# Optimization experiments

Hardware: AMD Instinct MI355X
Metric: run time of the kernel (lower is better)

The kernel has to match this reference:

```python
import jax, jax.numpy as jnp
import numpy as np

B, S, H, NH, HD = 2, 2048, 2048, 16, 128


def _bit_linear(x, w):
    """Ternary STE BitLinear: absmean scaling, round/clamp, fp matmul, rescale."""
    eps = 1e-5
    wn = w / (jnp.abs(w).mean() + eps)
    # straight-through estimator: forward uses quantized weights, grad flows to wn
    wq = wn + jax.lax.stop_gradient(jnp.clip(jnp.round(wn), -1.0, 1.0) - wn)
    y = x @ wq.T
    scale = w.shape[1]  # in_features
    Qb = 128.0  # 2**(8-1)
    return jnp.clip(y / scale * Qb, -Qb, Qb)


def _rotate_half(x):
    x1, x2 = jnp.split(x, 2, axis=-1)
    return jnp.concatenate([-x2, x1], axis=-1)


def setup_inputs() -> dict:
    key = jax.random.key(0)
    k1, k2, k3 = jax.random.split(key, 3)
    x = jax.random.normal(k1, (B, S, H), dtype=jnp.float32)
    w_qkv = jax.random.normal(k2, (3 * H, H), dtype=jnp.float32) * 0.02
    w_o = jax.random.normal(k3, (H, H), dtype=jnp.float32) * 0.02
    # realistic RoPE table [2, S, HD]
    inv_freq = 1.0 / (10000.0 ** (jnp.arange(0, HD, 2, dtype=jnp.float32) / HD))
    freqs = jnp.arange(S, dtype=jnp.float32)[:, None] * inv_freq[None, :]
    emb = jnp.concatenate([freqs, freqs], axis=-1)  # [S, HD]
    rotary = jnp.stack([jnp.cos(emb), jnp.sin(emb)], axis=0)
    return {"x": x, "rotary": rotary, "w_qkv": w_qkv, "w_o": w_o}


def reference(x, rotary, w_qkv, w_o):
    qkv = _bit_linear(x, w_qkv)  # [B, S, 3H]
    q, k, v = jnp.split(qkv, 3, axis=-1)
    q = q.reshape(B, S, NH, HD)
    k = k.reshape(B, S, NH, HD)
    v = v.reshape(B, S, NH, HD)
    cos = rotary[0][None, :, None, :]  # [1, S, 1, HD]
    sin = rotary[1][None, :, None, :]
    q = q * cos + _rotate_half(q) * sin
    k = k * cos + _rotate_half(k) * sin
    # [B, NH, S, HD]
    q, k, v = (t.transpose(0, 2, 1, 3) for t in (q, k, v))
    scores = jnp.einsum("bhqd,bhkd->bhqk", q, k) / np.sqrt(HD).astype(np.float32)
    causal = jnp.tril(jnp.ones((S, S), dtype=bool))
    scores = jnp.where(causal[None, None], scores, -jnp.inf)
    attn = jax.nn.softmax(scores, axis=-1)
    y = jnp.einsum("bhqk,bhkd->bhqd", attn, v)
    y = y.transpose(0, 2, 1, 3).reshape(B, S, H)
    return _bit_linear(y, w_o)
```

## Files before the change

### kernel.cpp

```cpp
#include <hip/hip_runtime.h>
#include <hip/hip_bf16.h>
#include <stdint.h>

#define B_   2
#define S_   2048
#define H_   2048
#define NH_  16
#define HD_  128
#define MTOK 4096
#define NQKV 6144

typedef unsigned short u16;
typedef __attribute__((ext_vector_type(8))) __bf16 bf16x8;
typedef __attribute__((ext_vector_type(4))) float f32x4;
typedef __attribute__((ext_vector_type(16))) float f32x16;

static __device__ __forceinline__ float bf2f(u16 u){
  union { uint32_t i; float f; } v; v.i = ((uint32_t)u) << 16; return v.f;
}
static __device__ __forceinline__ u16 f2bf(float f){
  union { float f; uint32_t i; } v; v.f = f;
  uint32_t r = v.i + 0x7FFFu + ((v.i >> 16) & 1u);
  return (u16)(r >> 16);
}
static __device__ __forceinline__ uint32_t cvt_pk_bf16(float lo, float hi){
  uint32_t r;
  asm("v_cvt_pk_bf16_f32 %0, %1, %2" : "=v"(r) : "v"(lo), "v"(hi));
  return r;
}
static __device__ __forceinline__ void pl32swap(uint32_t &a, uint32_t &b){
  asm volatile("v_permlane32_swap_b32 %0, %1" : "+v"(a), "+v"(b));
}

__device__ __forceinline__ void gload_lds16(const void* g, void* l){
  __builtin_amdgcn_global_load_lds((const __attribute__((address_space(1))) void*)g,
                                   (__attribute__((address_space(3))) void*)l, 16, 0, 0);
}

__global__ void absum_kernel(const float* __restrict__ w, int n, float* __restrict__ partial){
  __shared__ float sm[256];
  float s = 0.f;
  for (int i = blockIdx.x*256 + threadIdx.x; i < n; i += gridDim.x*256)
    s += fabsf(w[i]);
  sm[threadIdx.x] = s; __syncthreads();
  for (int st = 128; st > 0; st >>= 1){
    if ((int)threadIdx.x < st) sm[threadIdx.x] += sm[threadIdx.x + st];
    __syncthreads();
  }
  if (threadIdx.x == 0) partial[blockIdx.x] = sm[0];
}

__global__ void finalize_kernel(const float* __restrict__ p1, const float* __restrict__ p2,
                                float* __restrict__ scales){
  __shared__ double sm[256];
  int t = threadIdx.x;
  double s = (double)p1[t] + (double)p1[t+256] + (double)p1[t+512] + (double)p1[t+768];
  sm[t] = s; __syncthreads();
  for (int st = 128; st > 0; st >>= 1){ if (t < st) sm[t] += sm[t+st]; __syncthreads(); }
  if (t == 0) scales[0] = (float)(1.0 / (sm[0] / (double)(3*H_*H_) + 1e-5));
  __syncthreads();
  s = (double)p2[t] + (double)p2[t+256] + (double)p2[t+512] + (double)p2[t+768];
  sm[t] = s; __syncthreads();
  for (int st = 128; st > 0; st >>= 1){ if (t < st) sm[t] += sm[t+st]; __syncthreads(); }
  if (t == 0) scales[1] = (float)(1.0 / (sm[0] / (double)(H_*H_) + 1e-5));
}

__global__ void quantcast_kernel(const float* __restrict__ w_qkv, const float* __restrict__ w_o,
                                 const float* __restrict__ x, u16* __restrict__ wqkvq,
                                 u16* __restrict__ woq, u16* __restrict__ xb,
                                 const float* __restrict__ scales){
  const int n1 = 3*H_*H_, n2 = H_*H_, n3 = MTOK*H_;
  float inv0 = scales[0], inv1 = scales[1];
  for (int i = blockIdx.x*256 + threadIdx.x; i < n1 + n2 + n3; i += gridDim.x*256){
    if (i < n1){
      float q = rintf(w_qkv[i] * inv0);
      wqkvq[i] = f2bf(fminf(1.f, fmaxf(-1.f, q)));
    } else if (i < n1 + n2){
      int j = i - n1;
      float q = rintf(w_o[j] * inv1);
      woq[j] = f2bf(fminf(1.f, fmaxf(-1.f, q)));
    } else {
      int j = i - n1 - n2;
      xb[j] = f2bf(x[j]);
    }
  }
}

__global__ __launch_bounds__(512, 4) void gemmqkv_kernel(const u16* __restrict__ A,
    const u16* __restrict__ Bw, u16* __restrict__ qb, u16* __restrict__ kb, u16* __restrict__ vtb)
{
  const int M = MTOK, N = NQKV, K = H_;
  __shared__ u16 As[128*32];
  __shared__ u16 Bs[256*32];
  int nbn = N >> 8;
  int nb_tot = (M >> 7) * nbn;
  int bid = blockIdx.x;
  int chunk = nb_tot >> 3;
  bid = (bid & 7) * chunk + (bid >> 3);
  int bm = bid / nbn, bn = bid % nbn;
  int m0 = bm << 7, n0 = bn << 8;
  int tid = threadIdx.x;
  int lane = tid & 63, wid = tid >> 6;
  int wr = wid >> 2, wc = wid & 3;
  int lg = lane >> 4, lr = lane & 15;

  const u16* Ab = A + (size_t)m0 * K;
  const u16* Bb = Bw + (size_t)n0 * K;
  int srow = tid >> 2;
  int scol = (tid & 3) << 3;

  f32x4 acc[4][4];
  #pragma unroll
  for (int i = 0; i < 4; i++)
    #pragma unroll
    for (int j = 0; j < 4; j++) acc[i][j] = f32x4{0.f,0.f,0.f,0.f};

  for (int k0 = 0; k0 < K; k0 += 32){
    gload_lds16(Ab + (size_t)srow*K        + k0 + scol, As + tid*8);
    gload_lds16(Bb + (size_t)srow*K        + k0 + scol, Bs + tid*8);
    gload_lds16(Bb + (size_t)(srow+128)*K  + k0 + scol, Bs + 4096 + tid*8);
    __syncthreads();
    bf16x8 af[4], bfr[4];
    #pragma unroll
    for (int mi = 0; mi < 4; mi++) af[mi]  = *(const bf16x8*)(As + ((wr*64 + mi*16 + lr)*32 + lg*8));
    #pragma unroll
    for (int ni = 0; ni < 4; ni++) bfr[ni] = *(const bf16x8*)(Bs + ((wc*64 + ni*16 + lr)*32 + lg*8));
    #pragma unroll
    for (int mi = 0; mi < 4; mi++)
      #pragma unroll
      for (int ni = 0; ni < 4; ni++)
        acc[mi][ni] = __builtin_amdgcn_mfma_f32_16x16x32_bf16(af[mi], bfr[ni], acc[mi][ni], 0, 0, 0);
    __syncthreads();
  }

  #pragma unroll
  for (int mi = 0; mi < 4; mi++){
    #pragma unroll
    for (int ni = 0; ni < 4; ni++){
      int ncol = n0 + wc*64 + ni*16 + lr;
      #pragma unroll
      for (int r = 0; r < 4; r++){
        int m = m0 + wr*64 + mi*16 + lg*4 + r;
        float v = acc[mi][ni][r] * 0.0625f;
        v = fminf(128.f, fmaxf(-128.f, v));
        int b = m >> 11, s = m & 2047;
        int part = ncol >> 11, c = ncol & 2047;
        int h = c >> 7, d = c & 127;
        int bh = b*NH_ + h;
        u16 bv = f2bf(v);
        if (part == 0)      qb[((bh*S_ + s) << 7) + d] = bv;
        else if (part == 1) kb[((bh*S_ + s) << 7) + d] = bv;
        else                vtb[((bh*HD_ + d) << 11) + s] = bv;
      }
    }
  }
}

__global__ __launch_bounds__(256, 4) void gemmo_kernel(const u16* __restrict__ A,
    const u16* __restrict__ Bw, float* __restrict__ outf)
{
  const int M = MTOK, N = H_, K = H_;
  __shared__ u16 As[128*32];
  __shared__ u16 Bs[128*32];
  int nbn = N >> 7;
  int nb_tot = (M >> 7) * nbn;
  int bid = blockIdx.x;
  int chunk = nb_tot >> 3;
  bid = (bid & 7) * chunk + (bid >> 3);
  int bm = bid / nbn, bn = bid % nbn;
  int m0 = bm << 7, n0 = bn << 7;
  int tid = threadIdx.x;
  int lane = tid & 63, wid = tid >> 6;
  int wr = wid >> 1, wc = wid & 1;
  int lg = lane >> 4, lr = lane & 15;

  const u16* Ab = A + m0 * K;
  const u16* Bb = Bw + n0 * K;
  int srow = tid >> 2;
  int scol = (tid & 3) << 3;

  f32x4 acc[4][4];
  #pragma unroll
  for (int i = 0; i < 4; i++)
    #pragma unroll
    for (int j = 0; j < 4; j++) acc[i][j] = f32x4{0.f,0.f,0.f,0.f};

  for (int k0 = 0; k0 < K; k0 += 32){
    gload_lds16(Ab + srow*K      + k0 + scol, As + tid*8);
    gload_lds16(Ab + (srow+64)*K + k0 + scol, As + 2048 + tid*8);
    gload_lds16(Bb + srow*K      + k0 + scol, Bs + tid*8);
    gload_lds16(Bb + (srow+64)*K + k0 + scol, Bs + 2048 + tid*8);
    __syncthreads();
    bf16x8 af[4], bfr[4];
    #pragma unroll
    for (int mi = 0; mi < 4; mi++) af[mi]  = *(const bf16x8*)(As + ((wr*64 + mi*16 + lr)*32 + lg*8));
    #pragma unroll
    for (int ni = 0; ni < 4; ni++) bfr[ni] = *(const bf16x8*)(Bs + ((wc*64 + ni*16 + lr)*32 + lg*8));
    #pragma unroll
    for (int mi = 0; mi < 4; mi++)
      #pragma unroll
      for (int ni = 0; ni < 4; ni++)
        acc[mi][ni] = __builtin_amdgcn_mfma_f32_16x16x32_bf16(af[mi], bfr[ni], acc[mi][ni], 0, 0, 0);
    __syncthreads();
  }

  #pragma unroll
  for (int mi = 0; mi < 4; mi++){
    #pragma unroll
    for (int ni = 0; ni < 4; ni++){
      int ncol = n0 + wc*64 + ni*16 + lr;
      #pragma unroll
      for (int r = 0; r < 4; r++){
        int m = m0 + wr*64 + mi*16 + lg*4 + r;
        float v = acc[mi][ni][r] * 0.0625f;
        v = fminf(128.f, fmaxf(-128.f, v));
        outf[(size_t)m*N + ncol] = v;
      }
    }
  }
}

__global__ void rope_kernel(u16* __restrict__ qb, u16* __restrict__ kb, const float* __restrict__ rot){
  int i = blockIdx.x*256 + threadIdx.x;
  int d = i & 63;
  int s = (i >> 6) & 2047;
  int bh = (i >> 17) & 31;
  u16* buf = (i >> 22) ? kb : qb;
  int base = (bh*S_ + s)*HD_;
  float c  = rot[s*HD_ + d];
  float sn = rot[S_*HD_ + s*HD_ + d];
  float x1 = bf2f(buf[base + d]);
  float x2 = bf2f(buf[base + d + 64]);
  buf[base + d]      = f2bf(x1*c - x2*sn);
  buf[base + d + 64] = f2bf(x2*c + x1*sn);
}

__global__ __launch_bounds__(256) void attn_kernel(const u16* __restrict__ qb,
    const u16* __restrict__ kb, const u16* __restrict__ vtb, u16* __restrict__ ao)
{
  __shared__ alignas(16) u16 Ks[2][4096];
  __shared__ alignas(16) u16 Vs[2][4096];

  int bid = blockIdx.x;
  int sbid = (bid & 7)*64 + (bid >> 3);
  int bh = sbid >> 4;
  int bq = 15 - (sbid & 15);
  int tid = threadIdx.x;
  int wid = tid >> 6, lane = tid & 63;
  int l31 = lane & 31, hl = lane >> 5;
  int q0 = bq * 128;
  int qw = q0 + wid*32;
  int q  = qw + l31;

  const u16* Qp = qb + (size_t)(bh*S_ + qw)*HD_;
  const u16* Kp = kb + (size_t)bh*S_*HD_;
  const u16* Vt = vtb + (size_t)bh*HD_*S_;

  bf16x8 qf[8];
  #pragma unroll
  for (int t = 0; t < 8; t++)
    qf[t] = *(const bf16x8*)(Qp + l31*HD_ + t*16 + hl*8);

  f32x16 o[4];
  #pragma unroll
  for (int i = 0; i < 4; i++)
    #pragma unroll
    for (int j = 0; j < 16; j++) o[i][j] = 0.f;
  float m_r = -1e30f, l_r = 0.f;
  const float sm_scale = 0.08838834764831845f;

  auto STAGE = [&](int buf, int kt2){
    int t0 = wid*2;
    gload_lds16(Kp + (size_t)(kt2 + l31)*HD_ + (t0  )*16 + hl*8, &Ks[buf][((t0  )*64 + lane)*8]);
    gload_lds16(Kp + (size_t)(kt2 + l31)*HD_ + (t0+1)*16 + hl*8, &Ks[buf][((t0+1)*64 + lane)*8]);
    int v0 = wid*2, v1 = wid*2 + 1;
    gload_lds16(Vt + (size_t)((v0&3)*32 + l31)*S_ + kt2 + (v0>>2)*16 + hl*8, &Vs[buf][(v0*64 + lane)*8]);
    gload_lds16(Vt + (size_t)((v1&3)*32 + l31)*S_ + kt2 + (v1>>2)*16 + hl*8, &Vs[buf][(v1*64 + lane)*8]);
  };

  int n_it = 4*bq + 4;
  STAGE(0, 0);
  int cur = 0, kt = 0;
  for (int it = 0; it < n_it; ++it, kt += 32){
    if (it + 1 < n_it){
      STAGE(cur ^ 1, kt + 32);
      asm volatile("s_waitcnt vmcnt(4)" ::: "memory");
    } else {
      asm volatile("s_waitcnt vmcnt(0)" ::: "memory");
    }
    __builtin_amdgcn_sched_barrier(0);
    __builtin_amdgcn_s_barrier();

    if (kt <= qw){
      f32x16 sa;
      #pragma unroll
      for (int j = 0; j < 16; j++) sa[j] = 0.f;
      #pragma unroll
      for (int t = 0; t < 8; t++){
        bf16x8 kf = *(const bf16x8*)(&Ks[cur][(t*64 + lane)*8]);
        sa = __builtin_amdgcn_mfma_f32_32x32x16_bf16(kf, qf[t], sa, 0, 0, 0);
      }

      float sv[16];
      if (kt == qw){
        #pragma unroll
        for (int r = 0; r < 16; r++){
          int key = kt + (r&3) + 8*(r>>2) + 4*hl;
          sv[r] = (key > q) ? -1e30f : sa[r]*sm_scale;
        }
      } else {
        #pragma unroll
        for (int r = 0; r < 16; r++) sv[r] = sa[r]*sm_scale;
      }

      float pm = sv[0];
      #pragma unroll
      for (int r = 1; r < 16; r++) pm = fmaxf(pm, sv[r]);
      pm = fmaxf(pm, __shfl_xor(pm, 32));
      if (!__all(pm - m_r <= 8.f)){
        float mn = fmaxf(m_r, pm);
        float scl = __expf(m_r - mn);
        m_r = mn; l_r *= scl;
        #pragma unroll
        for (int i = 0; i < 4; i++)
          #pragma unroll
          for (int j = 0; j < 16; j++) o[i][j] *= scl;
      }
      float p[16];
      #pragma unroll
      for (int r = 0; r < 16; r++) p[r] = __expf(sv[r] - m_r);
      float ts = 0.f;
      #pragma unroll
      for (int r = 0; r < 16; r++) ts += p[r];
      ts += __shfl_xor(ts, 32);
      l_r += ts;

      uint32_t a0 = cvt_pk_bf16(p[0],  p[1]),  a1 = cvt_pk_bf16(p[2],  p[3]);
      uint32_t a2 = cvt_pk_bf16(p[4],  p[5]),  a3 = cvt_pk_bf16(p[6],  p[7]);
      uint32_t b0 = cvt_pk_bf16(p[8],  p[9]),  b1 = cvt_pk_bf16(p[10], p[11]);
      uint32_t b2 = cvt_pk_bf16(p[12], p[13]), b3 = cvt_pk_bf16(p[14], p[15]);
      pl32swap(a0, a2); pl32swap(a1, a3);
      pl32swap(b0, b2); pl32swap(b1, b3);
      union { uint32_t u[4]; bf16x8 v; } pf0, pf1;
      pf0.u[0]=a0; pf0.u[1]=a1; pf0.u[2]=a2; pf0.u[3]=a3;
      pf1.u[0]=b0; pf1.u[1]=b1; pf1.u[2]=b2; pf1.u[3]=b3;

      #pragma unroll
      for (int db = 0; db < 4; db++){
        bf16x8 vf0 = *(const bf16x8*)(&Vs[cur][((0*4 + db)*64 + lane)*8]);
        o[db] = __builtin_amdgcn_mfma_f32_32x32x16_bf16(vf0, pf0.v, o[db], 0, 0, 0);
        bf16x8 vf1 = *(const bf16x8*)(&Vs[cur][((1*4 + db)*64 + lane)*8]);
        o[db] = __builtin_amdgcn_mfma_f32_32x32x16_bf16(vf1, pf1.v, o[db], 0, 0, 0);
      }
      asm volatile("s_waitcnt lgkmcnt(0)" ::: "memory");
    }
    __builtin_amdgcn_sched_barrier(0);
    __builtin_amdgcn_s_barrier();
    cur ^= 1;
  }

  float inv = 1.f / l_r;
  int b = bh >> 4, hh = bh & 15;
  u16* orow = ao + (size_t)(b*S_ + q)*H_ + hh*HD_;
  #pragma unroll
  for (int db = 0; db < 4; db++){
    #pragma unroll
    for (int g = 0; g < 4; g++){
      ushort4 pk4;
      pk4.x = f2bf(o[db][4*g+0]*inv);
      pk4.y = f2bf(o[db][4*g+1]*inv);
      pk4.z = f2bf(o[db][4*g+2]*inv);
      pk4.w = f2bf(o[db][4*g+3]*inv);
      *(ushort4*)(orow + db*32 + g*8 + hl*4) = pk4;
    }
  }
}

extern "C" void kernel_launch(void* const* d_in, const int* in_sizes, int n_in,
                              void* d_out, int out_size, void* d_ws, size_t ws_size,
                              hipStream_t stream) {
  const float* x      = (const float*)d_in[0];
  const float* rotary = (const float*)d_in[1];
  const float* w_qkv  = (const float*)d_in[2];
  const float* w_o    = (const float*)d_in[3];
  float* out = (float*)d_out;

  char* wsb = (char*)d_ws;
  float* part_qkv = (float*)wsb;
  float* part_o   = part_qkv + 1024;
  float* scales   = part_o + 1024;
  size_t off = 16384;
  u16* xb    = (u16*)(wsb + off); off += (size_t)MTOK*H_*2;
  u16* wqkvq = (u16*)(wsb + off); off += (size_t)NQKV*H_*2;
  u16* woq   = (u16*)(wsb + off); off += (size_t)H_*H_*2;
  u16* qbuf  = (u16*)(wsb + off); off += (size_t)B_*NH_*S_*HD_*2;
  u16* kbuf  = (u16*)(wsb + off); off += (size_t)B_*NH_*S_*HD_*2;
  u16* vtb   = (u16*)(wsb + off); off += (size_t)B_*NH_*S_*HD_*2;
  u16* ao    = (u16*)(wsb + off); off += (size_t)MTOK*H_*2;

  absum_kernel<<<1024, 256, 0, stream>>>(w_qkv, 3*H_*H_, part_qkv);
  absum_kernel<<<1024, 256, 0, stream>>>(w_o, H_*H_, part_o);
  finalize_kernel<<<1, 256, 0, stream>>>(part_qkv, part_o, scales);
  quantcast_kernel<<<2048, 256, 0, stream>>>(w_qkv, w_o, x, wqkvq, woq, xb, scales);

  gemmqkv_kernel<<<(MTOK/128)*(NQKV/256), 512, 0, stream>>>(xb, wqkvq, qbuf, kbuf, vtb);
  rope_kernel<<<(2*B_*NH_*S_*64)/256, 256, 0, stream>>>(qbuf, kbuf, rotary);
  attn_kernel<<<B_*NH_*(S_/128), 256, 0, stream>>>(qbuf, kbuf, vtb, ao);
  gemmo_kernel<<<(MTOK/128)*(H_/128), 256, 0, stream>>>(ao, woq, out);
}
```

Baseline: 382.8 us.

## Double-buffer LDS tiles in QKV and output projection GEMMs

Both GEMM kernels now keep two LDS buffers and issue the global-to-LDS loads for the next K tile before computing on the current one. The aim is to overlap global memory latency with MFMA work and drop one barrier per iteration. It doubles shared memory per block, which may lower occupancy, and the single remaining barrier depends on how gload_lds completion is waited on (vmcnt) before the data is read.

```diff
diff --git a/kernel.cpp b/kernel.cpp
--- a/kernel.cpp
+++ b/kernel.cpp
@@ -90,8 +90,8 @@
     const u16* __restrict__ Bw, u16* __restrict__ qb, u16* __restrict__ kb, u16* __restrict__ vtb)
 {
   const int M = MTOK, N = NQKV, K = H_;
-  __shared__ u16 As[128*32];
-  __shared__ u16 Bs[256*32];
+  __shared__ u16 As[2][128*32];
+  __shared__ u16 Bs[2][256*32];
   int nbn = N >> 8;
   int nb_tot = (M >> 7) * nbn;
   int bid = blockIdx.x;
@@ -115,22 +115,30 @@
     #pragma unroll
     for (int j = 0; j < 4; j++) acc[i][j] = f32x4{0.f,0.f,0.f,0.f};
 
-  for (int k0 = 0; k0 < K; k0 += 32){
-    gload_lds16(Ab + (size_t)srow*K        + k0 + scol, As + tid*8);
-    gload_lds16(Bb + (size_t)srow*K        + k0 + scol, Bs + tid*8);
-    gload_lds16(Bb + (size_t)(srow+128)*K  + k0 + scol, Bs + 4096 + tid*8);
-    __syncthreads();
+  auto STAGE = [&](int buf, int k0){
+    gload_lds16(Ab + (size_t)srow*K       + k0 + scol, As[buf] + tid*8);
+    gload_lds16(Bb + (size_t)srow*K       + k0 + scol, Bs[buf] + tid*8);
+    gload_lds16(Bb + (size_t)(srow+128)*K + k0 + scol, Bs[buf] + 4096 + tid*8);
+  };
+
+  int NT = K >> 5;
+  STAGE(0, 0);
+  __syncthreads();
+  int buf = 0;
+  for (int t = 0; t < NT; t++){
+    if (t + 1 < NT) STAGE(buf ^ 1, (t + 1) << 5);
     bf16x8 af[4], bfr[4];
     #pragma unroll
-    for (int mi = 0; mi < 4; mi++) af[mi]  = *(const bf16x8*)(As + ((wr*64 + mi*16 + lr)*32 + lg*8));
-    #pragma unroll
-    for (int ni = 0; ni < 4; ni++) bfr[ni] = *(const bf16x8*)(Bs + ((wc*64 + ni*16 + lr)*32 + lg*8));
+    for (int mi = 0; mi < 4; mi++) af[mi]  = *(const bf16x8*)(As[buf] + ((wr*64 + mi*16 + lr)*32 + lg*8));
+    #pragma unroll
+    for (int ni = 0; ni < 4; ni++) bfr[ni] = *(const bf16x8*)(Bs[buf] + ((wc*64 + ni*16 + lr)*32 + lg*8));
     #pragma unroll
     for (int mi = 0; mi < 4; mi++)
       #pragma unroll
       for (int ni = 0; ni < 4; ni++)
         acc[mi][ni] = __builtin_amdgcn_mfma_f32_16x16x32_bf16(af[mi], bfr[ni], acc[mi][ni], 0, 0, 0);
     __syncthreads();
+    buf ^= 1;
   }
 
   #pragma unroll
@@ -160,8 +168,8 @@
     const u16* __restrict__ Bw, float* __restrict__ outf)
 {
   const int M = MTOK, N = H_, K = H_;
-  __shared__ u16 As[128*32];
-  __shared__ u16 Bs[128*32];
+  __shared__ u16 As[2][128*32];
+  __shared__ u16 Bs[2][128*32];
   int nbn = N >> 7;
   int nb_tot = (M >> 7) * nbn;
   int bid = blockIdx.x;
@@ -185,23 +193,31 @@
     #pragma unroll
     for (int j = 0; j < 4; j++) acc[i][j] = f32x4{0.f,0.f,0.f,0.f};
 
-  for (int k0 = 0; k0 < K; k0 += 32){
-    gload_lds16(Ab + srow*K      + k0 + scol, As + tid*8);
-    gload_lds16(Ab + (srow+64)*K + k0 + scol, As + 2048 + tid*8);
-    gload_lds16(Bb + srow*K      + k0 + scol, Bs + tid*8);
-    gload_lds16(Bb + (srow+64)*K + k0 + scol, Bs + 2048 + tid*8);
-    __syncthreads();
+  auto STAGE = [&](int buf, int k0){
+    gload_lds16(Ab + (size_t)srow*K      + k0 + scol, As[buf] + tid*8);
+    gload_lds16(Ab + (size_t)(srow+64)*K + k0 + scol, As[buf] + 2048 + tid*8);
+    gload_lds16(Bb + (size_t)srow*K      + k0 + scol, Bs[buf] + tid*8);
+    gload_lds16(Bb + (size_t)(srow+64)*K + k0 + scol, Bs[buf] + 2048 + tid*8);
+  };
+
+  int NT = K >> 5;
+  STAGE(0, 0);
+  __syncthreads();
+  int buf = 0;
+  for (int t = 0; t < NT; t++){
+    if (t + 1 < NT) STAGE(buf ^ 1, (t + 1) << 5);
     bf16x8 af[4], bfr[4];
     #pragma unroll
-    for (int mi = 0; mi < 4; mi++) af[mi]  = *(const bf16x8*)(As + ((wr*64 + mi*16 + lr)*32 + lg*8));
-    #pragma unroll
-    for (int ni = 0; ni < 4; ni++) bfr[ni] = *(const bf16x8*)(Bs + ((wc*64 + ni*16 + lr)*32 + lg*8));
+    for (int mi = 0; mi < 4; mi++) af[mi]  = *(const bf16x8*)(As[buf] + ((wr*64 + mi*16 + lr)*32 + lg*8));
+    #pragma unroll
+    for (int ni = 0; ni < 4; ni++) bfr[ni] = *(const bf16x8*)(Bs[buf] + ((wc*64 + ni*16 + lr)*32 + lg*8));
     #pragma unroll
     for (int mi = 0; mi < 4; mi++)
       #pragma unroll
       for (int ni = 0; ni < 4; ni++)
         acc[mi][ni] = __builtin_amdgcn_mfma_f32_16x16x32_bf16(af[mi], bfr[ni], acc[mi][ni], 0, 0, 0);
     __syncthreads();
+    buf ^= 1;
   }
 
   #pragma unroll
```

Measured after the change: 394.9 us. 3.1% more time.

## Double attention key tile to 64 per iteration and add MFMA priority hints

Applied to the files above, without the earlier changes.

The flash-attention kernel now stages 64 keys per iteration instead of 32, doubling the LDS buffers, and computes two 32x32 score tiles with a joint online-softmax update. This halves the number of barrier and wait round trips and softmax rescale checks per key. s_setprio is placed around the MFMA sections to favour matrix issue. In exchange it uses more LDS and registers per block, which may lower occupancy, and adds extra branching for the half-masked diagonal tile.

```diff
diff --git a/kernel.cpp b/kernel.cpp
--- a/kernel.cpp
+++ b/kernel.cpp
@@ -238,8 +238,8 @@
 __global__ __launch_bounds__(256) void attn_kernel(const u16* __restrict__ qb,
     const u16* __restrict__ kb, const u16* __restrict__ vtb, u16* __restrict__ ao)
 {
-  __shared__ alignas(16) u16 Ks[2][4096];
-  __shared__ alignas(16) u16 Vs[2][4096];
+  __shared__ alignas(16) u16 Ks[2][8192];
+  __shared__ alignas(16) u16 Vs[2][8192];
 
   int bid = blockIdx.x;
   int sbid = (bid & 7)*64 + (bid >> 3);
@@ -270,52 +270,65 @@
   const float sm_scale = 0.08838834764831845f;
 
   auto STAGE = [&](int buf, int kt2){
-    int t0 = wid*2;
-    gload_lds16(Kp + (size_t)(kt2 + l31)*HD_ + (t0  )*16 + hl*8, &Ks[buf][((t0  )*64 + lane)*8]);
-    gload_lds16(Kp + (size_t)(kt2 + l31)*HD_ + (t0+1)*16 + hl*8, &Ks[buf][((t0+1)*64 + lane)*8]);
-    int v0 = wid*2, v1 = wid*2 + 1;
-    gload_lds16(Vt + (size_t)((v0&3)*32 + l31)*S_ + kt2 + (v0>>2)*16 + hl*8, &Vs[buf][(v0*64 + lane)*8]);
-    gload_lds16(Vt + (size_t)((v1&3)*32 + l31)*S_ + kt2 + (v1>>2)*16 + hl*8, &Vs[buf][(v1*64 + lane)*8]);
+    #pragma unroll
+    for (int j = 0; j < 4; j++){
+      int f = wid*4 + j;
+      gload_lds16(Kp + (size_t)(kt2 + (f>>3)*32 + l31)*HD_ + (f&7)*16 + hl*8,
+                  &Ks[buf][f*512 + lane*8]);
+      gload_lds16(Vt + (size_t)((f&3)*32 + l31)*S_ + kt2 + (f>>2)*16 + hl*8,
+                  &Vs[buf][f*512 + lane*8]);
+    }
   };
 
-  int n_it = 4*bq + 4;
+  int n_it = 2*bq + 2;
   STAGE(0, 0);
   int cur = 0, kt = 0;
-  for (int it = 0; it < n_it; ++it, kt += 32){
+  for (int it = 0; it < n_it; ++it, kt += 64){
     if (it + 1 < n_it){
-      STAGE(cur ^ 1, kt + 32);
-      asm volatile("s_waitcnt vmcnt(4)" ::: "memory");
+      STAGE(cur ^ 1, kt + 64);
+      asm volatile("s_waitcnt vmcnt(8)" ::: "memory");
     } else {
       asm volatile("s_waitcnt vmcnt(0)" ::: "memory");
     }
     __builtin_amdgcn_sched_barrier(0);
     __builtin_amdgcn_s_barrier();
 
-    if (kt <= qw){
-      f32x16 sa;
-      #pragma unroll
-      for (int j = 0; j < 16; j++) sa[j] = 0.f;
+    if (kt < qw + 32){
+      bool half2 = kt < qw;
+      f32x16 sa0, sa1;
+      #pragma unroll
+      for (int j = 0; j < 16; j++){ sa0[j] = 0.f; sa1[j] = 0.f; }
+      __builtin_amdgcn_s_setprio(1);
       #pragma unroll
       for (int t = 0; t < 8; t++){
         bf16x8 kf = *(const bf16x8*)(&Ks[cur][(t*64 + lane)*8]);
-        sa = __builtin_amdgcn_mfma_f32_32x32x16_bf16(kf, qf[t], sa, 0, 0, 0);
-      }
-
-      float sv[16];
-      if (kt == qw){
+        sa0 = __builtin_amdgcn_mfma_f32_32x32x16_bf16(kf, qf[t], sa0, 0, 0, 0);
+      }
+      if (half2){
+        #pragma unroll
+        for (int t = 0; t < 8; t++){
+          bf16x8 kf = *(const bf16x8*)(&Ks[cur][((8 + t)*64 + lane)*8]);
+          sa1 = __builtin_amdgcn_mfma_f32_32x32x16_bf16(kf, qf[t], sa1, 0, 0, 0);
+        }
+      }
+      __builtin_amdgcn_s_setprio(0);
+
+      float sv[32];
+      if (kt + 63 <= qw){
+        #pragma unroll
+        for (int r = 0; r < 16; r++){ sv[r] = sa0[r]*sm_scale; sv[16+r] = sa1[r]*sm_scale; }
+      } else {
         #pragma unroll
         for (int r = 0; r < 16; r++){
-          int key = kt + (r&3) + 8*(r>>2) + 4*hl;
-          sv[r] = (key > q) ? -1e30f : sa[r]*sm_scale;
+          int crow = (r&3) + 8*(r>>2) + 4*hl;
+          sv[r]    = (kt + crow > q)               ? -1e30f : sa0[r]*sm_scale;
+          sv[16+r] = (!half2 || kt + 32 + crow > q) ? -1e30f : sa1[r]*sm_scale;
         }
-      } else {
-        #pragma unroll
-        for (int r = 0; r < 16; r++) sv[r] = sa[r]*sm_scale;
       }
 
       float pm = sv[0];
       #pragma unroll
-      for (int r = 1; r < 16; r++) pm = fmaxf(pm, sv[r]);
+      for (int r = 1; r < 32; r++) pm = fmaxf(pm, sv[r]);
       pm = fmaxf(pm, __shfl_xor(pm, 32));
       if (!__all(pm - m_r <= 8.f)){
         float mn = fmaxf(m_r, pm);
@@ -326,32 +339,44 @@
           #pragma unroll
           for (int j = 0; j < 16; j++) o[i][j] *= scl;
       }
-      float p[16];
-      #pragma unroll
-      for (int r = 0; r < 16; r++) p[r] = __expf(sv[r] - m_r);
+      float p[32];
+      #pragma unroll
+      for (int r = 0; r < 32; r++) p[r] = __expf(sv[r] - m_r);
       float ts = 0.f;
       #pragma unroll
-      for (int r = 0; r < 16; r++) ts += p[r];
+      for (int r = 0; r < 32; r++) ts += p[r];
       ts += __shfl_xor(ts, 32);
       l_r += ts;
 
-      uint32_t a0 = cvt_pk_bf16(p[0],  p[1]),  a1 = cvt_pk_bf16(p[2],  p[3]);
-      uint32_t a2 = cvt_pk_bf16(p[4],  p[5]),  a3 = cvt_pk_bf16(p[6],  p[7]);
-      uint32_t b0 = cvt_pk_bf16(p[8],  p[9]),  b1 = cvt_pk_bf16(p[10], p[11]);
-      uint32_t b2 = cvt_pk_bf16(p[12], p[13]), b3 = cvt_pk_bf16(p[14], p[15]);
-      pl32swap(a0, a2); pl32swap(a1, a3);
-      pl32swap(b0, b2); pl32swap(b1, b3);
-      union { uint32_t u[4]; bf16x8 v; } pf0, pf1;
-      pf0.u[0]=a0; pf0.u[1]=a1; pf0.u[2]=a2; pf0.u[3]=a3;
-      pf1.u[0]=b0; pf1.u[1]=b1; pf1.u[2]=b2; pf1.u[3]=b3;
-
+      union { uint32_t u[4]; bf16x8 v; } pf[4];
+      #pragma unroll
+      for (int g = 0; g < 4; g++){
+        uint32_t u0 = cvt_pk_bf16(p[8*g+0], p[8*g+1]);
+        uint32_t u1 = cvt_pk_bf16(p[8*g+2], p[8*g+3]);
+        uint32_t u2 = cvt_pk_bf16(p[8*g+4], p[8*g+5]);
+        uint32_t u3 = cvt_pk_bf16(p[8*g+6], p[8*g+7]);
+        pl32swap(u0, u2); pl32swap(u1, u3);
+        pf[g].u[0]=u0; pf[g].u[1]=u1; pf[g].u[2]=u2; pf[g].u[3]=u3;
+      }
+
+      __builtin_amdgcn_s_setprio(1);
       #pragma unroll
       for (int db = 0; db < 4; db++){
-        bf16x8 vf0 = *(const bf16x8*)(&Vs[cur][((0*4 + db)*64 + lane)*8]);
-        o[db] = __builtin_amdgcn_mfma_f32_32x32x16_bf16(vf0, pf0.v, o[db], 0, 0, 0);
-        bf16x8 vf1 = *(const bf16x8*)(&Vs[cur][((1*4 + db)*64 + lane)*8]);
-        o[db] = __builtin_amdgcn_mfma_f32_32x32x16_bf16(vf1, pf1.v, o[db], 0, 0, 0);
-      }
+        bf16x8 v0 = *(const bf16x8*)(&Vs[cur][((0*4 + db)*64 + lane)*8]);
+        o[db] = __builtin_amdgcn_mfma_f32_32x32x16_bf16(v0, pf[0].v, o[db], 0, 0, 0);
+        bf16x8 v1 = *(const bf16x8*)(&Vs[cur][((1*4 + db)*64 + lane)*8]);
+        o[db] = __builtin_amdgcn_mfma_f32_32x32x16_bf16(v1, pf[1].v, o[db], 0, 0, 0);
+      }
+      if (half2){
+        #pragma unroll
+        for (int db = 0; db < 4; db++){
+          bf16x8 v2 = *(const bf16x8*)(&Vs[cur][((2*4 + db)*64 + lane)*8]);
+          o[db] = __builtin_amdgcn_mfma_f32_32x32x16_bf16(v2, pf[2].v, o[db], 0, 0, 0);
+          bf16x8 v3 = *(const bf16x8*)(&Vs[cur][((3*4 + db)*64 + lane)*8]);
+          o[db] = __builtin_amdgcn_mfma_f32_32x32x16_bf16(v3, pf[3].v, o[db], 0, 0, 0);
+        }
+      }
+      __builtin_amdgcn_s_setprio(0);
       asm volatile("s_waitcnt lgkmcnt(0)" ::: "memory");
     }
     __builtin_amdgcn_sched_barrier(0);
```

Measured after the change: 421.4 us. 10.1% more time.

## Switch attention to 16x16x32 MFMA with 64-query blocks and doubled grid

Applied to the files above, without the earlier changes.

Rewrites the attention kernel to use 16x16x32 bf16 MFMA tiles, with each wave handling 16 queries and each block 64 queries, which doubles the number of blocks. Shuffles replace the permlane32 swap to rearrange P into the B-operand layout. The aim is finer causal granularity, less wasted diagonal work and better occupancy and load balance. In exchange, K/V tiles are loaded from global memory twice as often relative to the compute done, and the shuffles add cross-lane overhead.

```diff
diff --git a/kernel.cpp b/kernel.cpp
--- a/kernel.cpp
+++ b/kernel.cpp
@@ -13,7 +13,6 @@
 typedef unsigned short u16;
 typedef __attribute__((ext_vector_type(8))) __bf16 bf16x8;
 typedef __attribute__((ext_vector_type(4))) float f32x4;
-typedef __attribute__((ext_vector_type(16))) float f32x16;
 
 static __device__ __forceinline__ float bf2f(u16 u){
   union { uint32_t i; float f; } v; v.i = ((uint32_t)u) << 16; return v.f;
@@ -27,9 +26,6 @@
   uint32_t r;
   asm("v_cvt_pk_bf16_f32 %0, %1, %2" : "=v"(r) : "v"(lo), "v"(hi));
   return r;
-}
-static __device__ __forceinline__ void pl32swap(uint32_t &a, uint32_t &b){
-  asm volatile("v_permlane32_swap_b32 %0, %1" : "+v"(a), "+v"(b));
 }
 
 __device__ __forceinline__ void gload_lds16(const void* g, void* l){
@@ -242,43 +238,46 @@
   __shared__ alignas(16) u16 Vs[2][4096];
 
   int bid = blockIdx.x;
-  int sbid = (bid & 7)*64 + (bid >> 3);
-  int bh = sbid >> 4;
-  int bq = 15 - (sbid & 15);
+  int sbid = (bid & 7)*128 + (bid >> 3);
+  int bh = sbid >> 5;
+  int bq = 31 - (sbid & 31);
   int tid = threadIdx.x;
   int wid = tid >> 6, lane = tid & 63;
-  int l31 = lane & 31, hl = lane >> 5;
-  int q0 = bq * 128;
-  int qw = q0 + wid*32;
-  int q  = qw + l31;
+  int lg = lane >> 4, lr = lane & 15;
+  int q0 = bq * 64;
+  int qw = q0 + wid*16;
+  int q  = qw + lr;
 
   const u16* Qp = qb + (size_t)(bh*S_ + qw)*HD_;
   const u16* Kp = kb + (size_t)bh*S_*HD_;
   const u16* Vt = vtb + (size_t)bh*HD_*S_;
 
-  bf16x8 qf[8];
-  #pragma unroll
-  for (int t = 0; t < 8; t++)
-    qf[t] = *(const bf16x8*)(Qp + l31*HD_ + t*16 + hl*8);
-
-  f32x16 o[4];
-  #pragma unroll
-  for (int i = 0; i < 4; i++)
-    #pragma unroll
-    for (int j = 0; j < 16; j++) o[i][j] = 0.f;
+  bf16x8 qf[4];
+  #pragma unroll
+  for (int kk = 0; kk < 4; kk++)
+    qf[kk] = *(const bf16x8*)(Qp + lr*HD_ + kk*32 + lg*8);
+
+  f32x4 o[8];
+  #pragma unroll
+  for (int i = 0; i < 8; i++) o[i] = f32x4{0.f,0.f,0.f,0.f};
   float m_r = -1e30f, l_r = 0.f;
   const float sm_scale = 0.08838834764831845f;
 
+  int srcA = ((((lg&1)<<1) | (lg>>1)) << 4) + lr;
+  int srcB = srcA ^ 16;
+
   auto STAGE = [&](int buf, int kt2){
-    int t0 = wid*2;
-    gload_lds16(Kp + (size_t)(kt2 + l31)*HD_ + (t0  )*16 + hl*8, &Ks[buf][((t0  )*64 + lane)*8]);
-    gload_lds16(Kp + (size_t)(kt2 + l31)*HD_ + (t0+1)*16 + hl*8, &Ks[buf][((t0+1)*64 + lane)*8]);
-    int v0 = wid*2, v1 = wid*2 + 1;
-    gload_lds16(Vt + (size_t)((v0&3)*32 + l31)*S_ + kt2 + (v0>>2)*16 + hl*8, &Vs[buf][(v0*64 + lane)*8]);
-    gload_lds16(Vt + (size_t)((v1&3)*32 + l31)*S_ + kt2 + (v1>>2)*16 + hl*8, &Vs[buf][(v1*64 + lane)*8]);
+    #pragma unroll
+    for (int j = 0; j < 2; j++){
+      int f = wid*2 + j;
+      gload_lds16(Kp + (size_t)(kt2 + (f>>2)*16 + lr)*HD_ + (f&3)*32 + lg*8,
+                  &Ks[buf][(f*64 + lane)*8]);
+      gload_lds16(Vt + (size_t)(f*16 + lr)*S_ + kt2 + lg*8,
+                  &Vs[buf][(f*64 + lane)*8]);
+    }
   };
 
-  int n_it = 4*bq + 4;
+  int n_it = 2*bq + 2;
   STAGE(0, 0);
   int cur = 0, kt = 0;
   for (int it = 0; it < n_it; ++it, kt += 32){
@@ -291,66 +290,71 @@
     __builtin_amdgcn_sched_barrier(0);
     __builtin_amdgcn_s_barrier();
 
-    if (kt <= qw){
-      f32x16 sa;
-      #pragma unroll
-      for (int j = 0; j < 16; j++) sa[j] = 0.f;
-      #pragma unroll
-      for (int t = 0; t < 8; t++){
-        bf16x8 kf = *(const bf16x8*)(&Ks[cur][(t*64 + lane)*8]);
-        sa = __builtin_amdgcn_mfma_f32_32x32x16_bf16(kf, qf[t], sa, 0, 0, 0);
-      }
-
-      float sv[16];
-      if (kt == qw){
+    if (kt <= qw + 15){
+      f32x4 s0 = f32x4{0.f,0.f,0.f,0.f}, s1 = f32x4{0.f,0.f,0.f,0.f};
+      #pragma unroll
+      for (int kk = 0; kk < 4; kk++){
+        bf16x8 ka  = *(const bf16x8*)(&Ks[cur][((kk    )*64 + lane)*8]);
+        bf16x8 kb2 = *(const bf16x8*)(&Ks[cur][((4 + kk)*64 + lane)*8]);
+        s0 = __builtin_amdgcn_mfma_f32_16x16x32_bf16(ka,  qf[kk], s0, 0, 0, 0);
+        s1 = __builtin_amdgcn_mfma_f32_16x16x32_bf16(kb2, qf[kk], s1, 0, 0, 0);
+      }
+
+      float sv[8];
+      if (kt + 31 <= qw){
         #pragma unroll
-        for (int r = 0; r < 16; r++){
-          int key = kt + (r&3) + 8*(r>>2) + 4*hl;
-          sv[r] = (key > q) ? -1e30f : sa[r]*sm_scale;
-        }
+        for (int r = 0; r < 4; r++){ sv[r] = s0[r]*sm_scale; sv[4+r] = s1[r]*sm_scale; }
       } else {
         #pragma unroll
-        for (int r = 0; r < 16; r++) sv[r] = sa[r]*sm_scale;
-      }
-
-      float pm = sv[0];
-      #pragma unroll
-      for (int r = 1; r < 16; r++) pm = fmaxf(pm, sv[r]);
+        for (int r = 0; r < 4; r++){
+          sv[r]   = (kt + 4*lg + r      > q) ? -1e30f : s0[r]*sm_scale;
+          sv[4+r] = (kt + 16 + 4*lg + r > q) ? -1e30f : s1[r]*sm_scale;
+        }
+      }
+
+      float pm = fmaxf(fmaxf(fmaxf(sv[0],sv[1]), fmaxf(sv[2],sv[3])),
+                       fmaxf(fmaxf(sv[4],sv[5]), fmaxf(sv[6],sv[7])));
+      pm = fmaxf(pm, __shfl_xor(pm, 16));
       pm = fmaxf(pm, __shfl_xor(pm, 32));
       if (!__all(pm - m_r <= 8.f)){
         float mn = fmaxf(m_r, pm);
         float scl = __expf(m_r - mn);
         m_r = mn; l_r *= scl;
         #pragma unroll
-        for (int i = 0; i < 4; i++)
+        for (int i = 0; i < 8; i++)
           #pragma unroll
-          for (int j = 0; j < 16; j++) o[i][j] *= scl;
-      }
-      float p[16];
-      #pragma unroll
-      for (int r = 0; r < 16; r++) p[r] = __expf(sv[r] - m_r);
-      float ts = 0.f;
-      #pragma unroll
-      for (int r = 0; r < 16; r++) ts += p[r];
+          for (int j = 0; j < 4; j++) o[i][j] *= scl;
+      }
+      float p[8];
+      #pragma unroll
+      for (int i = 0; i < 8; i++) p[i] = __expf(sv[i] - m_r);
+      float ts = ((p[0]+p[1]) + (p[2]+p[3])) + ((p[4]+p[5]) + (p[6]+p[7]));
+      ts += __shfl_xor(ts, 16);
       ts += __shfl_xor(ts, 32);
       l_r += ts;
 
-      uint32_t a0 = cvt_pk_bf16(p[0],  p[1]),  a1 = cvt_pk_bf16(p[2],  p[3]);
-      uint32_t a2 = cvt_pk_bf16(p[4],  p[5]),  a3 = cvt_pk_bf16(p[6],  p[7]);
-      uint32_t b0 = cvt_pk_bf16(p[8],  p[9]),  b1 = cvt_pk_bf16(p[10], p[11]);
-      uint32_t b2 = cvt_pk_bf16(p[12], p[13]), b3 = cvt_pk_bf16(p[14], p[15]);
-      pl32swap(a0, a2); pl32swap(a1, a3);
-      pl32swap(b0, b2); pl32swap(b1, b3);
-      union { uint32_t u[4]; bf16x8 v; } pf0, pf1;
-      pf0.u[0]=a0; pf0.u[1]=a1; pf0.u[2]=a2; pf0.u[3]=a3;
-      pf1.u[0]=b0; pf1.u[1]=b1; pf1.u[2]=b2; pf1.u[3]=b3;
-
-      #pragma unroll
-      for (int db = 0; db < 4; db++){
-        bf16x8 vf0 = *(const bf16x8*)(&Vs[cur][((0*4 + db)*64 + lane)*8]);
-        o[db] = __builtin_amdgcn_mfma_f32_32x32x16_bf16(vf0, pf0.v, o[db], 0, 0, 0);
-        bf16x8 vf1 = *(const bf16x8*)(&Vs[cur][((1*4 + db)*64 + lane)*8]);
-        o[db] = __builtin_amdgcn_mfma_f32_32x32x16_bf16(vf1, pf1.v, o[db], 0, 0, 0);
+      uint32_t w0 = cvt_pk_bf16(p[0], p[1]);
+      uint32_t w1 = cvt_pk_bf16(p[2], p[3]);
+      uint32_t w2 = cvt_pk_bf16(p[4], p[5]);
+      uint32_t w3 = cvt_pk_bf16(p[6], p[7]);
+      uint32_t e0 = (lg & 1) ? w2 : w0;
+      uint32_t e1 = (lg & 1) ? w0 : w2;
+      uint32_t e2 = (lg & 1) ? w3 : w1;
+      uint32_t e3 = (lg & 1) ? w1 : w3;
+      uint32_t r0 = (uint32_t)__shfl((int)e0, srcA, 64);
+      uint32_t r1 = (uint32_t)__shfl((int)e1, srcB, 64);
+      uint32_t r2 = (uint32_t)__shfl((int)e2, srcA, 64);
+      uint32_t r3 = (uint32_t)__shfl((int)e3, srcB, 64);
+      union { uint32_t u[4]; bf16x8 v; } pu;
+      pu.u[0] = (lg < 2) ? r0 : r1;
+      pu.u[1] = (lg < 2) ? r2 : r3;
+      pu.u[2] = (lg < 2) ? r1 : r0;
+      pu.u[3] = (lg < 2) ? r3 : r2;
+
+      #pragma unroll
+      for (int db = 0; db < 8; db++){
+        bf16x8 vf = *(const bf16x8*)(&Vs[cur][(db*64 + lane)*8]);
+        o[db] = __builtin_amdgcn_mfma_f32_16x16x32_bf16(vf, pu.v, o[db], 0, 0, 0);
       }
       asm volatile("s_waitcnt lgkmcnt(0)" ::: "memory");
     }
@@ -363,16 +367,13 @@
   int b = bh >> 4, hh = bh & 15;
   u16* orow = ao + (size_t)(b*S_ + q)*H_ + hh*HD_;
   #pragma unroll
-  for (int db = 0; db < 4; db++){
-    #pragma unroll
-    for (int g = 0; g < 4; g++){
-      ushort4 pk4;
-      pk4.x = f2bf(o[db][4*g+0]*inv);
-      pk4.y = f2bf(o[db][4*g+1]*inv);
-      pk4.z = f2bf(o[db][4*g+2]*inv);
-      pk4.w = f2bf(o[db][4*g+3]*inv);
-      *(ushort4*)(orow + db*32 + g*8 + hl*4) = pk4;
-    }
+  for (int db = 0; db < 8; db++){
+    ushort4 pk;
+    pk.x = f2bf(o[db][0]*inv);
+    pk.y = f2bf(o[db][1]*inv);
+    pk.z = f2bf(o[db][2]*inv);
+    pk.w = f2bf(o[db][3]*inv);
+    *(ushort4*)(orow + db*16 + lg*4) = pk;
   }
 }
 
@@ -405,6 +406,6 @@
 
   gemmqkv_kernel<<<(MTOK/128)*(NQKV/256), 512, 0, stream>>>(xb, wqkvq, qbuf, kbuf, vtb);
   rope_kernel<<<(2*B_*NH_*S_*64)/256, 256, 0, stream>>>(qbuf, kbuf, rotary);
-  attn_kernel<<<B_*NH_*(S_/128), 256, 0, stream>>>(qbuf, kbuf, vtb, ao);
+  attn_kernel<<<B_*NH_*(S_/64), 256, 0, stream>>>(qbuf, kbuf, vtb, ao);
   gemmo_kernel<<<(MTOK/128)*(H_/128), 256, 0, stream>>>(ao, woq, out);
 }
```

New measurement: 398.4 us. +4.1%, slower.
